# Optimization experiments

Measured on AMD Instinct MI355X. Metric: run time of the kernel, lower is better.

Reference implementation:

```python
import jax, jax.numpy as jnp
import numpy as np

B, T, H, K = 128, 4096, 128, 5


def logistic_logcdf(x, mean, log_scale):
    z = (x - mean) * jnp.exp(-log_scale)
    return jax.nn.log_sigmoid(z)


def logistic_logpdf(x, mean, log_scale):
    z = (x - mean) * jnp.exp(-log_scale)
    zh = z / 2
    return -2 * jnp.logaddexp(zh, -zh) - log_scale


def mixlogistic_logcdf(x, prior_logits, means, log_scales):
    x = x[..., None]
    log_pi = jax.nn.log_softmax(prior_logits, axis=-1)
    return jax.nn.logsumexp(log_pi + logistic_logcdf(x, means, log_scales), axis=-1)


def mixlogistic_logpdf(x, prior_logits, means, log_scales):
    x = x[..., None]
    log_pi = jax.nn.log_softmax(prior_logits, axis=-1)
    return jax.nn.logsumexp(log_pi + logistic_logpdf(x, means, log_scales), axis=-1)


def coupling_function(x, pi, mu, log_s):
    log_cdf = jnp.minimum(mixlogistic_logcdf(x, pi, mu, log_s), -1e-12)
    log_1m = jnp.log(-jnp.expm1(log_cdf))
    val = log_cdf - log_1m
    log_jac = mixlogistic_logpdf(x, pi, mu, log_s) - log_cdf - log_1m
    return val, log_jac


def gru_step(h, x, Wi, Wh, bi, bhn):
    # flax GRUCell: input denses have bias, hidden denses no bias except hn.
    gi = x @ Wi + bi                      # [B, 3H]
    gh = h @ Wh                           # [B, 3H]
    ir, iz, inn = jnp.split(gi, 3, axis=-1)
    hr, hz, hn = jnp.split(gh, 3, axis=-1)
    r = jax.nn.sigmoid(ir + hr)
    z = jax.nn.sigmoid(iz + hz)
    n = jnp.tanh(inn + r * (hn + bhn))
    return (1.0 - z) * n + z * h


def setup_inputs() -> dict:
    key = jax.random.key(0)
    ks = jax.random.split(key, 14)
    g = lambda i, shape: (jax.random.normal(ks[i], shape) * 0.08).astype(jnp.float32)
    return {
        's': jax.random.normal(ks[0], (B, T), jnp.float32),
        'x': jax.random.normal(ks[1], (B, T), jnp.float32),
        'eps': jax.random.logistic(ks[2], (B, T), jnp.float32),
        # encoder GRU (in_features=1)
        'Wi_e': g(3, (1, 3 * H)), 'Wh_e': g(4, (H, 3 * H)),
        'bi_e': jnp.zeros(3 * H, jnp.float32), 'bhn_e': jnp.zeros(H, jnp.float32),
        # decoder GRU (in_features=1+H)
        'Wi_d': g(5, (1 + H, 3 * H)), 'Wh_d': g(6, (H, 3 * H)),
        'bi_d': jnp.zeros(3 * H, jnp.float32), 'bhn_d': jnp.zeros(H, jnp.float32),
        # heads
        'W_shift': g(7, (H, 1)), 'b_shift': jnp.zeros(1, jnp.float32),
        'W_lsc': g(8, (H, 1)), 'b_lsc': jnp.zeros(1, jnp.float32),
        'W_pi': g(9, (H, K)), 'b_pi': jnp.zeros(K, jnp.float32),
        'W_mu': g(10, (H, K)), 'b_mu': jnp.zeros(K, jnp.float32),
        'W_ls': g(11, (H, K)), 'b_ls': jnp.zeros(K, jnp.float32),
    }


def reference(s, x, eps, Wi_e, Wh_e, bi_e, bhn_e, Wi_d, Wh_d, bi_d, bhn_d,
              W_shift, b_shift, W_lsc, b_lsc, W_pi, b_pi, W_mu, b_mu, W_ls, b_ls):
    Bn, Tn = s.shape
    Hn = Wh_e.shape[0]
    s3 = s[..., None]  # [B,T,1]
    x3 = x[..., None]

    # --- encoder: reverse GRU, outputs kept in scan (reversed) order ---
    def enc_step(h, xt):
        h = gru_step(h, xt, Wi_e, Wh_e, bi_e, bhn_e)
        return h, h

    x_rev = jnp.flip(x3, axis=1).transpose(1, 0, 2)  # [T,B,1]
    _, h_x = jax.lax.scan(enc_step, jnp.zeros((Bn, Hn), s.dtype), x_rev)
    h_x = h_x.transpose(1, 0, 2)  # [B,T,H]

    sc = jnp.concatenate([s3, h_x], axis=-1)  # [B,T,1+H]

    def dec_step(carry, xs_t):
        h, pred = carry
        inp, e = xs_t              # inp [B,1+H], e [B]
        inp = inp.at[:, 0].set(pred)
        h = gru_step(h, inp, Wi_d, Wh_d, bi_d, bhn_d)
        y = h
        shift = (y @ W_shift + b_shift)[:, 0]
        log_scale = (y @ W_lsc + b_lsc)[:, 0]
        pi = y @ W_pi + b_pi
        mu = y @ W_mu + b_mu
        log_s = y @ W_ls + b_ls
        val, log_jac = coupling_function(e, pi, mu, log_s)
        prediction = shift + val * jnp.exp(log_scale)
        # standard logistic logpdf(e) = -e - 2*softplus(-e)
        logp = (-e - 2 * jax.nn.softplus(-e)) - log_scale - log_jac
        return (h, prediction), (logp, prediction)

    carry0 = (jnp.zeros((Bn, Hn), s.dtype), jnp.zeros(Bn, s.dtype))
    xs = (sc.transpose(1, 0, 2), eps.T)
    _, (logp, preds) = jax.lax.scan(dec_step, carry0, xs)
    return logp.T, preds.T  # each [B,T]
```

## Files before the change

kernel.cpp:

```cpp
#include <hip/hip_runtime.h>
#include <hip/hip_fp16.h>

#define Tn 4096
#define Bn 128
#define Hn 128
#define G3 384
#define NTH 448

typedef unsigned short u16;
typedef unsigned int u32;
typedef _Float16 f16;
typedef _Float16 h2 __attribute__((ext_vector_type(2)));

__device__ __forceinline__ float sigm(float v) { return 1.f / (1.f + __expf(-v)); }
__device__ __forceinline__ float tanh_fast(float v) {
  v = fminf(fmaxf(v, -15.f), 15.f);
  float e = __expf(-2.f * v);
  return (1.f - e) / (1.f + e);
}
__device__ __forceinline__ u16 f2h(float f) { return __half_as_ushort(__float2half(f)); }
__device__ __forceinline__ float h2f(u16 u) { return __half2float(__ushort_as_half(u)); }
__device__ __forceinline__ h2 bch2(u32 v) { union { u32 u; h2 h; } t; t.u = v; return t.h; }
__device__ __forceinline__ u32 bcu32(h2 v) { union { u32 u; h2 h; } t; t.h = v; return t.u; }
__device__ __forceinline__ float fdot2f(h2 a, h2 b, float c) {
  return __builtin_amdgcn_fdot2(a, b, c, false);
}

__global__ __launch_bounds__(NTH, 1) void combo_kernel(
    const float* __restrict__ x, const float* __restrict__ Wi_e,
    const float* __restrict__ Wh_e, const float* __restrict__ bi_e,
    const float* __restrict__ bhn_e, u16* __restrict__ hx,
    float* __restrict__ enc_h,
    const float* __restrict__ eps, const float* __restrict__ Wi_d,
    const float* __restrict__ Wh_d, const float* __restrict__ bhn_d,
    const float* __restrict__ W_shift, const float* __restrict__ b_shift,
    const float* __restrict__ W_lsc, const float* __restrict__ b_lsc,
    const float* __restrict__ W_pi, const float* __restrict__ b_pi,
    const float* __restrict__ W_mu, const float* __restrict__ b_mu,
    const float* __restrict__ W_ls, const float* __restrict__ b_ls,
    const u16* __restrict__ gi_pre, float* __restrict__ out,
    float* __restrict__ dec_h, float* __restrict__ dec_pred,
    int enc_t0, int dec_t0, int Tc)
{
  const int j = threadIdx.x;
  __shared__ __align__(16) f16 Xp[Hn];
  __shared__ __align__(16) float g2[512];
  __shared__ __align__(16) u32 hwlp[17 * 68];
  __shared__ float hbias_l[20];
  __shared__ float pred_s;
  const int bid = blockIdx.x;
  const int jj = (j < 384) ? j : 0;

  if (bid < Bn) {
    if (enc_t0 < 0) return;
    const int b = bid, t0 = enc_t0;
    h2 wp[64];
#pragma unroll
    for (int k = 0; k < 64; ++k) {
      h2 t; t.x = (f16)Wh_e[(2 * k) * G3 + jj]; t.y = (f16)Wh_e[(2 * k + 1) * G3 + jj];
      wp[k] = t;
    }
    float wie = 0.f, bie = 0.f, bhn = 0.f, hm = 0.f;
    if (j < 384) { wie = Wi_e[j]; bie = bi_e[j]; }
    if (j < Hn) {
      bhn = bhn_e[j];
      hm = (t0 == 0) ? 0.f : enc_h[(long)b * Hn + j];
      Xp[j] = (f16)hm;
    }
    __syncthreads();
    const float* xrow = x + (long)b * Tn;
    u16* hxrow = hx + (long)b * Tc * Hn;
    float xt = xrow[Tn - 1 - t0];
    for (int tt = 0; tt < Tc; ++tt) {
      const int t = t0 + tt;
      const int tnext = (t + 1 < Tn) ? (t + 1) : (Tn - 1);
      float xnext = xrow[Tn - 1 - tnext];
      if (j < 384) {
        const uint4* hp = (const uint4*)Xp;
        float a0 = 0.f, a1 = 0.f, a2 = 0.f, a3 = 0.f;
#pragma unroll
        for (int q = 0; q < 16; ++q) {
          uint4 hv = hp[q];
          a0 = fdot2f(bch2(hv.x), wp[4 * q + 0], a0);
          a1 = fdot2f(bch2(hv.y), wp[4 * q + 1], a1);
          a2 = fdot2f(bch2(hv.z), wp[4 * q + 2], a2);
          a3 = fdot2f(bch2(hv.w), wp[4 * q + 3], a3);
        }
        float gh = (a0 + a1) + (a2 + a3);
        float gi = fmaf(xt, wie, bie);
        if (j < 256) g2[j] = gh + gi;
        else { g2[j] = gh; g2[j + 128] = gi; }
      }
      __syncthreads();
      if (j < Hn) {
        float r = sigm(g2[j]);
        float z = sigm(g2[128 + j]);
        float n = tanh_fast(g2[384 + j] + r * (g2[256 + j] + bhn));
        float hn2 = (1.f - z) * n + z * hm;
        hm = hn2;
        Xp[j] = (f16)hn2;
        hxrow[(long)tt * Hn + j] = f2h(hn2);
      }
      xt = xnext;
      __syncthreads();
    }
    if (j < Hn) enc_h[(long)b * Hn + j] = hm;
  } else {
    if (dec_t0 < 0) return;
    const int b = bid - Bn, t0 = dec_t0;
    h2 wp[64];
#pragma unroll
    for (int k = 0; k < 64; ++k) {
      h2 t; t.x = (f16)Wh_d[(2 * k) * G3 + jj]; t.y = (f16)Wh_d[(2 * k + 1) * G3 + jj];
      wp[k] = t;
    }
    float bhn = 0.f, wr0 = 0.f, wz0 = 0.f, wn0 = 0.f, hm = 0.f;
    if (j < Hn) {
      bhn = bhn_d[j];
      wr0 = Wi_d[j];
      wz0 = Wi_d[128 + j];
      wn0 = Wi_d[256 + j];
      hm = (t0 == 0) ? 0.f : dec_h[(long)b * Hn + j];
      Xp[j] = (f16)hm;
    }
    for (int idx = j; idx < 17 * 64; idx += NTH) {
      int o = idx >> 6, k2 = idx & 63;
      int ka = 2 * k2, kb = 2 * k2 + 1;
      float wa, wb;
      if (o == 0) { wa = W_shift[ka]; wb = W_shift[kb]; }
      else if (o == 1) { wa = W_lsc[ka]; wb = W_lsc[kb]; }
      else if (o < 7) { wa = W_pi[ka * 5 + o - 2]; wb = W_pi[kb * 5 + o - 2]; }
      else if (o < 12) { wa = W_mu[ka * 5 + o - 7]; wb = W_mu[kb * 5 + o - 7]; }
      else { wa = W_ls[ka * 5 + o - 12]; wb = W_ls[kb * 5 + o - 12]; }
      h2 t; t.x = (f16)wa; t.y = (f16)wb;
      hwlp[o * 68 + k2] = bcu32(t);
    }
    if (j < 17)
      hbias_l[j] = (j == 0) ? b_shift[0] : (j == 1) ? b_lsc[0] : (j < 7) ? b_pi[j - 2]
                 : (j < 12) ? b_mu[j - 7] : b_ls[j - 12];
    float predreg = (t0 == 0) ? 0.f : dec_pred[b];
    if (j == 384) pred_s = predreg;
    const u16* girow = gi_pre + (long)b * Tc * G3 + jj;
    const float* erow = eps + (long)b * Tn;
    float e_cur = erow[t0];
    u16 gA = 0, gB = 0;
    if (j < 384) { gA = girow[0]; gB = girow[(Tc > 1) ? G3 : 0]; }
    __syncthreads();
    const int lane = j - 384;
    const int ho = lane >> 1, hs = lane & 1;
    float* outlp = out + (long)b * Tn + t0;
    float* outpr = out + (long)Bn * Tn + (long)b * Tn + t0;
    for (int i = 0; i <= Tc; ++i) {
      u16 gC = 0; float e_next = 0.f;
      if (j < 384 && i < Tc) {
        int ip = (i + 2 < Tc) ? i + 2 : Tc - 1;
        gC = girow[(long)ip * G3];
      }
      if (j >= 384 && i < Tc) e_next = erow[t0 + i];
      if (j < 384) {
        if (i < Tc) {
          const uint4* hp = (const uint4*)Xp;
          float a0 = 0.f, a1 = 0.f, a2 = 0.f, a3 = 0.f;
#pragma unroll
          for (int q = 0; q < 16; ++q) {
            uint4 hv = hp[q];
            a0 = fdot2f(bch2(hv.x), wp[4 * q + 0], a0);
            a1 = fdot2f(bch2(hv.y), wp[4 * q + 1], a1);
            a2 = fdot2f(bch2(hv.z), wp[4 * q + 2], a2);
            a3 = fdot2f(bch2(hv.w), wp[4 * q + 3], a3);
          }
          float gh = (a0 + a1) + (a2 + a3);
          float gipre = h2f(gA);
          if (j < 256) g2[j] = gh + gipre;
          else { g2[j] = gh; g2[j + 128] = gipre; }
        }
      } else if (i >= 1) {
        float p = 0.f;
        if (lane < 34) {
          const uint4* hp4 = (const uint4*)Xp;
          const uint4* wr4 = (const uint4*)&hwlp[ho * 68 + hs * 32];
#pragma unroll
          for (int q = 0; q < 8; ++q) {
            uint4 hv = hp4[hs * 8 + q];
            uint4 wv = wr4[q];
            p = fdot2f(bch2(hv.x), bch2(wv.x), p);
            p = fdot2f(bch2(hv.y), bch2(wv.y), p);
            p = fdot2f(bch2(hv.z), bch2(wv.z), p);
            p = fdot2f(bch2(hv.w), bch2(wv.w), p);
          }
        }
        p += __shfl_xor(p, 1);
        float pb = p + hbias_l[lane < 34 ? ho : 0];
        const int lj2 = lane & 7;
        float pi_ = __shfl(pb, 4 + 2 * lj2);
        float mu_ = __shfl(pb, 14 + 2 * lj2);
        float ls_ = __shfl(pb, 24 + 2 * lj2);
        float shiftv = __shfl(pb, 0);
        float lscv = __shfl(pb, 2);
        const bool valid = (lane < 5);
        const float e = e_cur;
        float wexp = valid ? __expf(pi_) : 0.f;
        float zz = (e - mu_) * __expf(-ls_);
        float u = __expf(-fabsf(zz));
        float d = 1.f / (1.f + u);
        float sigp = (zz >= 0.f) ? d : u * d;
        float sigq = (zz >= 0.f) ? u * d : d;
        float pdfl = u * d * d * __expf(-ls_);
        float c = wexp * sigp, m = wexp * sigq, pp = wexp * pdfl, S = wexp;
        c += __shfl_xor(c, 1, 8); m += __shfl_xor(m, 1, 8);
        pp += __shfl_xor(pp, 1, 8); S += __shfl_xor(S, 1, 8);
        c += __shfl_xor(c, 2, 8); m += __shfl_xor(m, 2, 8);
        pp += __shfl_xor(pp, 2, 8); S += __shfl_xor(S, 2, 8);
        c += __shfl_xor(c, 4, 8); m += __shfl_xor(m, 4, 8);
        pp += __shfl_xor(pp, 4, 8); S += __shfl_xor(S, 4, 8);
        if (lane == 0) {
          float logc = __logf(c), logm = __logf(m);
          float val = logc - logm;
          float ljac = __logf(pp) + __logf(S) - logc - logm;
          float prednew = fmaf(val, __expf(lscv), shiftv);
          float sp = fmaxf(-e, 0.f) + log1pf(__expf(-fabsf(e)));
          float logp = (-e - 2.f * sp) - lscv - ljac;
          outlp[i - 1] = logp;
          outpr[i - 1] = prednew;
          pred_s = prednew;
          predreg = prednew;
        }
      }
      __syncthreads();
      if (j < Hn && i < Tc) {
        float pred = pred_s;
        float r = sigm(fmaf(pred, wr0, g2[j]));
        float z = sigm(fmaf(pred, wz0, g2[128 + j]));
        float n = tanh_fast(fmaf(pred, wn0, g2[384 + j]) + r * (g2[256 + j] + bhn));
        float hn2 = (1.f - z) * n + z * hm;
        hm = hn2;
        Xp[j] = (f16)hn2;
      }
      __syncthreads();
      gA = gB; gB = gC; e_cur = e_next;
    }
    if (j < Hn) dec_h[(long)b * Hn + j] = hm;
    if (j == 384) dec_pred[b] = predreg;
  }
}

__global__ __launch_bounds__(256) void gemm_gi(
    const u16* __restrict__ A, const float* __restrict__ Wi_d,
    const float* __restrict__ bi_d, u16* __restrict__ C)
{
  __shared__ __align__(16) float As[16][64];
  __shared__ __align__(16) float Ws[16][64];
  const int tid = threadIdx.x;
  const long m0 = (long)blockIdx.x * 64;
  const int n0 = blockIdx.y * 64;
  const int tx = tid & 15, ty = tid >> 4;
  const int am = tid >> 2, ak = (tid & 3) * 4;
  const int wk = tid >> 4, wn = (tid & 15) * 4;
  float acc[4][4] = {};
  for (int k0 = 0; k0 < Hn; k0 += 16) {
    uint2 a2v = *(const uint2*)(A + (m0 + am) * Hn + k0 + ak);
    float4 w4 = *(const float4*)(Wi_d + (long)(1 + k0 + wk) * G3 + n0 + wn);
    __syncthreads();
    As[ak + 0][am] = h2f((u16)(a2v.x & 0xffffu));
    As[ak + 1][am] = h2f((u16)(a2v.x >> 16));
    As[ak + 2][am] = h2f((u16)(a2v.y & 0xffffu));
    As[ak + 3][am] = h2f((u16)(a2v.y >> 16));
    *(float4*)&Ws[wk][wn] = w4;
    __syncthreads();
#pragma unroll
    for (int kk = 0; kk < 16; ++kk) {
      float4 av = *(const float4*)&As[kk][ty * 4];
      float4 wv = *(const float4*)&Ws[kk][tx * 4];
      float ar[4] = {av.x, av.y, av.z, av.w};
      float wr[4] = {wv.x, wv.y, wv.z, wv.w};
#pragma unroll
      for (int i = 0; i < 4; ++i)
#pragma unroll
        for (int jj = 0; jj < 4; ++jj) acc[i][jj] = fmaf(ar[i], wr[jj], acc[i][jj]);
    }
  }
  const float4 bb = *(const float4*)(bi_d + n0 + tx * 4);
  const float br[4] = {bb.x, bb.y, bb.z, bb.w};
#pragma unroll
  for (int i = 0; i < 4; ++i) {
    long row = m0 + ty * 4 + i;
    u32 lo = (u32)f2h(acc[i][0] + br[0]) | ((u32)f2h(acc[i][1] + br[1]) << 16);
    u32 hi = (u32)f2h(acc[i][2] + br[2]) | ((u32)f2h(acc[i][3] + br[3]) << 16);
    uint2 o; o.x = lo; o.y = hi;
    *(uint2*)(C + row * G3 + n0 + tx * 4) = o;
  }
}

extern "C" void kernel_launch(void* const* d_in, const int* in_sizes, int n_in,
                              void* d_out, int out_size, void* d_ws, size_t ws_size,
                              hipStream_t stream) {
  const float* x = (const float*)d_in[1];
  const float* eps = (const float*)d_in[2];
  const float* Wi_e = (const float*)d_in[3];
  const float* Wh_e = (const float*)d_in[4];
  const float* bi_e = (const float*)d_in[5];
  const float* bhn_e = (const float*)d_in[6];
  const float* Wi_d = (const float*)d_in[7];
  const float* Wh_d = (const float*)d_in[8];
  const float* bi_d = (const float*)d_in[9];
  const float* bhn_d = (const float*)d_in[10];
  const float* W_shift = (const float*)d_in[11];
  const float* b_shift = (const float*)d_in[12];
  const float* W_lsc = (const float*)d_in[13];
  const float* b_lsc = (const float*)d_in[14];
  const float* W_pi = (const float*)d_in[15];
  const float* b_pi = (const float*)d_in[16];
  const float* W_mu = (const float*)d_in[17];
  const float* b_mu = (const float*)d_in[18];
  const float* W_ls = (const float*)d_in[19];
  const float* b_ls = (const float*)d_in[20];
  float* out = (float*)d_out;

  const size_t stateB = (size_t)(2 * Bn * Hn + Bn) * sizeof(float);
  const size_t stateAl = (stateB + 255) & ~(size_t)255;
  int Tc = 512;
  while (Tc > 8 && stateAl + (size_t)Bn * Tc * (Hn + G3) * 2 > ws_size) Tc >>= 1;
  if (stateAl + (size_t)Bn * Tc * (Hn + G3) * 2 > ws_size) return;

  float* enc_h = (float*)d_ws;
  float* dec_h = enc_h + (size_t)Bn * Hn;
  float* dec_pred = dec_h + (size_t)Bn * Hn;
  u16* hx = (u16*)((char*)d_ws + stateAl);
  u16* gi = hx + (size_t)Bn * Tc * Hn;

  const int Nc = Tn / Tc;
  const dim3 gg((unsigned)(((size_t)Bn * Tc) / 64), G3 / 64);
  for (int k = 0; k <= Nc; ++k) {
    int enc_t0 = (k < Nc) ? k * Tc : -1;
    int dec_t0 = (k >= 1) ? (k - 1) * Tc : -1;
    combo_kernel<<<2 * Bn, NTH, 0, stream>>>(
        x, Wi_e, Wh_e, bi_e, bhn_e, hx, enc_h,
        eps, Wi_d, Wh_d, bhn_d, W_shift, b_shift, W_lsc, b_lsc,
        W_pi, b_pi, W_mu, b_mu, W_ls, b_ls,
        gi, out, dec_h, dec_pred, enc_t0, dec_t0, Tc);
    if (k < Nc) gemm_gi<<<gg, 256, 0, stream>>>(hx, Wi_d, bi_d, gi);
  }
}
```

Before: 6.230 ms.

## Transpose hx and gi buffers to time-major per feature and batch sequential loads by eight

The encoder hidden-state buffer and the precomputed decoder input-gate buffer are stored time-contiguous per (batch, feature) instead of feature-contiguous per timestep. Encoder and decoder loops now run in chunks of 8 steps, so each thread does one 16-byte load or store per 8 steps for x, eps, hx, gi and outputs, rather than scattered 2-byte and 4-byte accesses every step. The GEMM is adapted to read and write the transposed layouts. This adds register pressure from the unrolled 8-step bodies and raises the minimum chunk size to 64.

```diff
diff --git a/kernel.cpp b/kernel.cpp
--- a/kernel.cpp
+++ b/kernel.cpp
@@ -38,7 +38,7 @@
     const float* __restrict__ W_pi, const float* __restrict__ b_pi,
     const float* __restrict__ W_mu, const float* __restrict__ b_mu,
     const float* __restrict__ W_ls, const float* __restrict__ b_ls,
-    const u16* __restrict__ gi_pre, float* __restrict__ out,
+    const u16* __restrict__ gi2, float* __restrict__ out,
     float* __restrict__ dec_h, float* __restrict__ dec_pred,
     int enc_t0, int dec_t0, int Tc)
 {
@@ -67,42 +67,64 @@
       hm = (t0 == 0) ? 0.f : enc_h[(long)b * Hn + j];
       Xp[j] = (f16)hm;
     }
+    const float* xrow = x + (long)b * Tn;
+    u16* hxrow2 = hx + ((long)b * Hn + (j < Hn ? j : 0)) * Tc;
+    float xc0, xc1, xc2, xc3, xc4, xc5, xc6, xc7;
+    {
+      int base = Tn - 8 - t0; if (base < 0) base = 0;
+      float4 v0 = *(const float4*)(xrow + base), v1 = *(const float4*)(xrow + base + 4);
+      xc0 = v1.w; xc1 = v1.z; xc2 = v1.y; xc3 = v1.x;
+      xc4 = v0.w; xc5 = v0.z; xc6 = v0.y; xc7 = v0.x;
+    }
     __syncthreads();
-    const float* xrow = x + (long)b * Tn;
-    u16* hxrow = hx + (long)b * Tc * Hn;
-    float xt = xrow[Tn - 1 - t0];
-    for (int tt = 0; tt < Tc; ++tt) {
-      const int t = t0 + tt;
-      const int tnext = (t + 1 < Tn) ? (t + 1) : (Tn - 1);
-      float xnext = xrow[Tn - 1 - tnext];
-      if (j < 384) {
-        const uint4* hp = (const uint4*)Xp;
-        float a0 = 0.f, a1 = 0.f, a2 = 0.f, a3 = 0.f;
-#pragma unroll
-        for (int q = 0; q < 16; ++q) {
-          uint4 hv = hp[q];
-          a0 = fdot2f(bch2(hv.x), wp[4 * q + 0], a0);
-          a1 = fdot2f(bch2(hv.y), wp[4 * q + 1], a1);
-          a2 = fdot2f(bch2(hv.z), wp[4 * q + 2], a2);
-          a3 = fdot2f(bch2(hv.w), wp[4 * q + 3], a3);
+    for (int i8 = 0; i8 < Tc; i8 += 8) {
+      int nbase = Tn - 8 - t0 - (i8 + 8); if (nbase < 0) nbase = 0;
+      float4 nv0 = *(const float4*)(xrow + nbase);
+      float4 nv1 = *(const float4*)(xrow + nbase + 4);
+      u32 hb0_ = 0, hb1_ = 0, hb2_ = 0, hb3_ = 0;
+#pragma unroll
+      for (int u = 0; u < 8; ++u) {
+        const float xt = (u == 0) ? xc0 : (u == 1) ? xc1 : (u == 2) ? xc2
+                        : (u == 3) ? xc3 : (u == 4) ? xc4 : (u == 5) ? xc5
+                        : (u == 6) ? xc6 : xc7;
+        if (j < 384) {
+          const uint4* hp = (const uint4*)Xp;
+          float a0 = 0.f, a1 = 0.f, a2 = 0.f, a3 = 0.f;
+#pragma unroll
+          for (int q = 0; q < 16; ++q) {
+            uint4 hv = hp[q];
+            a0 = fdot2f(bch2(hv.x), wp[4 * q + 0], a0);
+            a1 = fdot2f(bch2(hv.y), wp[4 * q + 1], a1);
+            a2 = fdot2f(bch2(hv.z), wp[4 * q + 2], a2);
+            a3 = fdot2f(bch2(hv.w), wp[4 * q + 3], a3);
+          }
+          float gh = (a0 + a1) + (a2 + a3);
+          float gi = fmaf(xt, wie, bie);
+          if (j < 256) g2[j] = gh + gi;
+          else { g2[j] = gh; g2[j + 128] = gi; }
         }
-        float gh = (a0 + a1) + (a2 + a3);
-        float gi = fmaf(xt, wie, bie);
-        if (j < 256) g2[j] = gh + gi;
-        else { g2[j] = gh; g2[j + 128] = gi; }
-      }
-      __syncthreads();
+        __syncthreads();
+        if (j < Hn) {
+          float r = sigm(g2[j]);
+          float z = sigm(g2[128 + j]);
+          float n = tanh_fast(g2[384 + j] + r * (g2[256 + j] + bhn));
+          float hn2 = (1.f - z) * n + z * hm;
+          hm = hn2;
+          Xp[j] = (f16)hn2;
+          u16 hv = f2h(hn2);
+          if (u == 0) hb0_ = hv; else if (u == 1) hb0_ |= ((u32)hv << 16);
+          else if (u == 2) hb1_ = hv; else if (u == 3) hb1_ |= ((u32)hv << 16);
+          else if (u == 4) hb2_ = hv; else if (u == 5) hb2_ |= ((u32)hv << 16);
+          else if (u == 6) hb3_ = hv; else hb3_ |= ((u32)hv << 16);
+        }
+        __syncthreads();
+      }
       if (j < Hn) {
-        float r = sigm(g2[j]);
-        float z = sigm(g2[128 + j]);
-        float n = tanh_fast(g2[384 + j] + r * (g2[256 + j] + bhn));
-        float hn2 = (1.f - z) * n + z * hm;
-        hm = hn2;
-        Xp[j] = (f16)hn2;
-        hxrow[(long)tt * Hn + j] = f2h(hn2);
-      }
-      xt = xnext;
-      __syncthreads();
+        uint4 o; o.x = hb0_; o.y = hb1_; o.z = hb2_; o.w = hb3_;
+        *(uint4*)(hxrow2 + i8) = o;
+      }
+      xc0 = nv1.w; xc1 = nv1.z; xc2 = nv1.y; xc3 = nv1.x;
+      xc4 = nv0.w; xc5 = nv0.z; xc6 = nv0.y; xc7 = nv0.x;
     }
     if (j < Hn) enc_h[(long)b * Hn + j] = hm;
   } else {
@@ -140,25 +162,87 @@
                  : (j < 12) ? b_mu[j - 7] : b_ls[j - 12];
     float predreg = (t0 == 0) ? 0.f : dec_pred[b];
     if (j == 384) pred_s = predreg;
-    const u16* girow = gi_pre + (long)b * Tc * G3 + jj;
+    const u16* girow2 = gi2 + ((long)b * G3 + jj) * Tc;
     const float* erow = eps + (long)b * Tn;
-    float e_cur = erow[t0];
-    u16 gA = 0, gB = 0;
-    if (j < 384) { gA = girow[0]; gB = girow[(Tc > 1) ? G3 : 0]; }
+    uint4 gA4 = {0, 0, 0, 0};
+    float ep = 0.f, ec0 = 0, ec1 = 0, ec2 = 0, ec3 = 0, ec4 = 0, ec5 = 0, ec6 = 0, ec7 = 0;
+    if (j < 384) {
+      gA4 = *(const uint4*)(girow2);
+    } else {
+      float4 v0 = *(const float4*)(erow + t0), v1 = *(const float4*)(erow + t0 + 4);
+      ec0 = v0.x; ec1 = v0.y; ec2 = v0.z; ec3 = v0.w;
+      ec4 = v1.x; ec5 = v1.y; ec6 = v1.z; ec7 = v1.w;
+    }
+    float lp0 = 0, lp1 = 0, lp2 = 0, lp3 = 0, lp4 = 0, lp5 = 0, lp6 = 0, lp7 = 0;
+    float pr0 = 0, pr1 = 0, pr2 = 0, pr3 = 0, pr4 = 0, pr5 = 0, pr6 = 0, pr7 = 0;
     __syncthreads();
     const int lane = j - 384;
     const int ho = lane >> 1, hs = lane & 1;
     float* outlp = out + (long)b * Tn + t0;
     float* outpr = out + (long)Bn * Tn + (long)b * Tn + t0;
-    for (int i = 0; i <= Tc; ++i) {
-      u16 gC = 0; float e_next = 0.f;
-      if (j < 384 && i < Tc) {
-        int ip = (i + 2 < Tc) ? i + 2 : Tc - 1;
-        gC = girow[(long)ip * G3];
-      }
-      if (j >= 384 && i < Tc) e_next = erow[t0 + i];
+
+    auto couple = [&](float e) -> float2 {
+      float p = 0.f;
+      if (lane < 34) {
+        const uint4* hp4 = (const uint4*)Xp;
+        const uint4* wr4 = (const uint4*)&hwlp[ho * 68 + hs * 32];
+#pragma unroll
+        for (int q = 0; q < 8; ++q) {
+          uint4 hv = hp4[hs * 8 + q];
+          uint4 wv = wr4[q];
+          p = fdot2f(bch2(hv.x), bch2(wv.x), p);
+          p = fdot2f(bch2(hv.y), bch2(wv.y), p);
+          p = fdot2f(bch2(hv.z), bch2(wv.z), p);
+          p = fdot2f(bch2(hv.w), bch2(wv.w), p);
+        }
+      }
+      p += __shfl_xor(p, 1);
+      float pb = p + hbias_l[lane < 34 ? ho : 0];
+      const int lj2 = lane & 7;
+      float pi_ = __shfl(pb, 4 + 2 * lj2);
+      float mu_ = __shfl(pb, 14 + 2 * lj2);
+      float ls_ = __shfl(pb, 24 + 2 * lj2);
+      float shiftv = __shfl(pb, 0);
+      float lscv = __shfl(pb, 2);
+      const bool valid = (lane < 5);
+      float wexp = valid ? __expf(pi_) : 0.f;
+      float zz = (e - mu_) * __expf(-ls_);
+      float uq = __expf(-fabsf(zz));
+      float dq = 1.f / (1.f + uq);
+      float sigp = (zz >= 0.f) ? dq : uq * dq;
+      float sigq = (zz >= 0.f) ? uq * dq : dq;
+      float pdfl = uq * dq * dq * __expf(-ls_);
+      float c = wexp * sigp, m = wexp * sigq, pq = wexp * pdfl, S = wexp;
+      c += __shfl_xor(c, 1, 8); m += __shfl_xor(m, 1, 8);
+      pq += __shfl_xor(pq, 1, 8); S += __shfl_xor(S, 1, 8);
+      c += __shfl_xor(c, 2, 8); m += __shfl_xor(m, 2, 8);
+      pq += __shfl_xor(pq, 2, 8); S += __shfl_xor(S, 2, 8);
+      c += __shfl_xor(c, 4, 8); m += __shfl_xor(m, 4, 8);
+      pq += __shfl_xor(pq, 4, 8); S += __shfl_xor(S, 4, 8);
+      float logc = __logf(c), logm = __logf(m);
+      float val = logc - logm;
+      float ljac = __logf(pq) + __logf(S) - logc - logm;
+      float prednew = fmaf(val, __expf(lscv), shiftv);
+      float sp = fmaxf(-e, 0.f) + log1pf(__expf(-fabsf(e)));
+      float logp = (-e - 2.f * sp) - lscv - ljac;
+      return make_float2(logp, prednew);
+    };
+
+    for (int i8 = 0; i8 < Tc; i8 += 8) {
+      uint4 gB4 = {0, 0, 0, 0};
+      float4 en0 = {0, 0, 0, 0}, en1 = {0, 0, 0, 0};
       if (j < 384) {
-        if (i < Tc) {
+        int gn = i8 + 8; if (gn > Tc - 8) gn = Tc - 8;
+        gB4 = *(const uint4*)(girow2 + gn);
+      } else {
+        int sn = t0 + i8 + 8; if (sn > Tn - 8) sn = Tn - 8;
+        en0 = *(const float4*)(erow + sn);
+        en1 = *(const float4*)(erow + sn + 4);
+      }
+#pragma unroll
+      for (int u = 0; u < 8; ++u) {
+        const int i = i8 + u;
+        if (j < 384) {
           const uint4* hp = (const uint4*)Xp;
           float a0 = 0.f, a1 = 0.f, a2 = 0.f, a3 = 0.f;
 #pragma unroll
@@ -170,74 +254,64 @@
             a3 = fdot2f(bch2(hv.w), wp[4 * q + 3], a3);
           }
           float gh = (a0 + a1) + (a2 + a3);
-          float gipre = h2f(gA);
+          u16 gv = (u == 0) ? (u16)gA4.x : (u == 1) ? (u16)(gA4.x >> 16)
+                 : (u == 2) ? (u16)gA4.y : (u == 3) ? (u16)(gA4.y >> 16)
+                 : (u == 4) ? (u16)gA4.z : (u == 5) ? (u16)(gA4.z >> 16)
+                 : (u == 6) ? (u16)gA4.w : (u16)(gA4.w >> 16);
+          float gipre = h2f(gv);
           if (j < 256) g2[j] = gh + gipre;
           else { g2[j] = gh; g2[j + 128] = gipre; }
-        }
-      } else if (i >= 1) {
-        float p = 0.f;
-        if (lane < 34) {
-          const uint4* hp4 = (const uint4*)Xp;
-          const uint4* wr4 = (const uint4*)&hwlp[ho * 68 + hs * 32];
-#pragma unroll
-          for (int q = 0; q < 8; ++q) {
-            uint4 hv = hp4[hs * 8 + q];
-            uint4 wv = wr4[q];
-            p = fdot2f(bch2(hv.x), bch2(wv.x), p);
-            p = fdot2f(bch2(hv.y), bch2(wv.y), p);
-            p = fdot2f(bch2(hv.z), bch2(wv.z), p);
-            p = fdot2f(bch2(hv.w), bch2(wv.w), p);
+        } else if (i >= 1) {
+          float e = (u == 0) ? ep : (u == 1) ? ec0 : (u == 2) ? ec1 : (u == 3) ? ec2
+                  : (u == 4) ? ec3 : (u == 5) ? ec4 : (u == 6) ? ec5 : ec6;
+          float2 rr = couple(e);
+          if (lane == 0) {
+            if (u == 0) { lp7 = rr.x; pr7 = rr.y; }
+            else if (u == 1) { lp0 = rr.x; pr0 = rr.y; }
+            else if (u == 2) { lp1 = rr.x; pr1 = rr.y; }
+            else if (u == 3) { lp2 = rr.x; pr2 = rr.y; }
+            else if (u == 4) { lp3 = rr.x; pr3 = rr.y; }
+            else if (u == 5) { lp4 = rr.x; pr4 = rr.y; }
+            else if (u == 6) { lp5 = rr.x; pr5 = rr.y; }
+            else { lp6 = rr.x; pr6 = rr.y; }
+            pred_s = rr.y;
+            predreg = rr.y;
+            if (u == 0 && i8 > 0) {
+              *(float4*)(outlp + i8 - 8) = make_float4(lp0, lp1, lp2, lp3);
+              *(float4*)(outlp + i8 - 4) = make_float4(lp4, lp5, lp6, lp7);
+              *(float4*)(outpr + i8 - 8) = make_float4(pr0, pr1, pr2, pr3);
+              *(float4*)(outpr + i8 - 4) = make_float4(pr4, pr5, pr6, pr7);
+            }
           }
         }
-        p += __shfl_xor(p, 1);
-        float pb = p + hbias_l[lane < 34 ? ho : 0];
-        const int lj2 = lane & 7;
-        float pi_ = __shfl(pb, 4 + 2 * lj2);
-        float mu_ = __shfl(pb, 14 + 2 * lj2);
-        float ls_ = __shfl(pb, 24 + 2 * lj2);
-        float shiftv = __shfl(pb, 0);
-        float lscv = __shfl(pb, 2);
-        const bool valid = (lane < 5);
-        const float e = e_cur;
-        float wexp = valid ? __expf(pi_) : 0.f;
-        float zz = (e - mu_) * __expf(-ls_);
-        float u = __expf(-fabsf(zz));
-        float d = 1.f / (1.f + u);
-        float sigp = (zz >= 0.f) ? d : u * d;
-        float sigq = (zz >= 0.f) ? u * d : d;
-        float pdfl = u * d * d * __expf(-ls_);
-        float c = wexp * sigp, m = wexp * sigq, pp = wexp * pdfl, S = wexp;
-        c += __shfl_xor(c, 1, 8); m += __shfl_xor(m, 1, 8);
-        pp += __shfl_xor(pp, 1, 8); S += __shfl_xor(S, 1, 8);
-        c += __shfl_xor(c, 2, 8); m += __shfl_xor(m, 2, 8);
-        pp += __shfl_xor(pp, 2, 8); S += __shfl_xor(S, 2, 8);
-        c += __shfl_xor(c, 4, 8); m += __shfl_xor(m, 4, 8);
-        pp += __shfl_xor(pp, 4, 8); S += __shfl_xor(S, 4, 8);
-        if (lane == 0) {
-          float logc = __logf(c), logm = __logf(m);
-          float val = logc - logm;
-          float ljac = __logf(pp) + __logf(S) - logc - logm;
-          float prednew = fmaf(val, __expf(lscv), shiftv);
-          float sp = fmaxf(-e, 0.f) + log1pf(__expf(-fabsf(e)));
-          float logp = (-e - 2.f * sp) - lscv - ljac;
-          outlp[i - 1] = logp;
-          outpr[i - 1] = prednew;
-          pred_s = prednew;
-          predreg = prednew;
+        __syncthreads();
+        if (j < Hn) {
+          float pred = pred_s;
+          float r = sigm(fmaf(pred, wr0, g2[j]));
+          float z = sigm(fmaf(pred, wz0, g2[128 + j]));
+          float n = tanh_fast(fmaf(pred, wn0, g2[384 + j]) + r * (g2[256 + j] + bhn));
+          float hn2 = (1.f - z) * n + z * hm;
+          hm = hn2;
+          Xp[j] = (f16)hn2;
         }
-      }
-      __syncthreads();
-      if (j < Hn && i < Tc) {
-        float pred = pred_s;
-        float r = sigm(fmaf(pred, wr0, g2[j]));
-        float z = sigm(fmaf(pred, wz0, g2[128 + j]));
-        float n = tanh_fast(fmaf(pred, wn0, g2[384 + j]) + r * (g2[256 + j] + bhn));
-        float hn2 = (1.f - z) * n + z * hm;
-        hm = hn2;
-        Xp[j] = (f16)hn2;
-      }
-      __syncthreads();
-      gA = gB; gB = gC; e_cur = e_next;
+        __syncthreads();
+      }
+      gA4 = gB4;
+      if (j >= 384) {
+        ep = ec7;
+        ec0 = en0.x; ec1 = en0.y; ec2 = en0.z; ec3 = en0.w;
+        ec4 = en1.x; ec5 = en1.y; ec6 = en1.z; ec7 = en1.w;
+      }
+    }
+    if (j >= 384) {
+      float2 rr = couple(ep);
+      if (lane == 0) {
+        lp7 = rr.x; pr7 = rr.y; predreg = rr.y;
+        *(float4*)(outlp + Tc - 8) = make_float4(lp0, lp1, lp2, lp3);
+        *(float4*)(outlp + Tc - 4) = make_float4(lp4, lp5, lp6, lp7);
+        *(float4*)(outpr + Tc - 8) = make_float4(pr0, pr1, pr2, pr3);
+        *(float4*)(outpr + Tc - 4) = make_float4(pr4, pr5, pr6, pr7);
+      }
     }
     if (j < Hn) dec_h[(long)b * Hn + j] = hm;
     if (j == 384) dec_pred[b] = predreg;
@@ -245,26 +319,28 @@
 }
 
 __global__ __launch_bounds__(256) void gemm_gi(
-    const u16* __restrict__ A, const float* __restrict__ Wi_d,
-    const float* __restrict__ bi_d, u16* __restrict__ C)
+    const u16* __restrict__ A2, const float* __restrict__ Wi_d,
+    const float* __restrict__ bi_d, u16* __restrict__ C2, int Tc)
 {
   __shared__ __align__(16) float As[16][64];
   __shared__ __align__(16) float Ws[16][64];
   const int tid = threadIdx.x;
   const long m0 = (long)blockIdx.x * 64;
   const int n0 = blockIdx.y * 64;
+  const int bb = (int)(m0 / Tc);
+  const int tt0 = (int)(m0 - (long)bb * Tc);
   const int tx = tid & 15, ty = tid >> 4;
-  const int am = tid >> 2, ak = (tid & 3) * 4;
+  const int lk = tid >> 4, lm = (tid & 15) * 4;
   const int wk = tid >> 4, wn = (tid & 15) * 4;
   float acc[4][4] = {};
   for (int k0 = 0; k0 < Hn; k0 += 16) {
-    uint2 a2v = *(const uint2*)(A + (m0 + am) * Hn + k0 + ak);
+    uint2 a2v = *(const uint2*)(A2 + ((long)bb * Hn + k0 + lk) * Tc + tt0 + lm);
     float4 w4 = *(const float4*)(Wi_d + (long)(1 + k0 + wk) * G3 + n0 + wn);
     __syncthreads();
-    As[ak + 0][am] = h2f((u16)(a2v.x & 0xffffu));
-    As[ak + 1][am] = h2f((u16)(a2v.x >> 16));
-    As[ak + 2][am] = h2f((u16)(a2v.y & 0xffffu));
-    As[ak + 3][am] = h2f((u16)(a2v.y >> 16));
+    As[lk][lm + 0] = h2f((u16)(a2v.x & 0xffffu));
+    As[lk][lm + 1] = h2f((u16)(a2v.x >> 16));
+    As[lk][lm + 2] = h2f((u16)(a2v.y & 0xffffu));
+    As[lk][lm + 3] = h2f((u16)(a2v.y >> 16));
     *(float4*)&Ws[wk][wn] = w4;
     __syncthreads();
 #pragma unroll
@@ -279,15 +355,15 @@
         for (int jj = 0; jj < 4; ++jj) acc[i][jj] = fmaf(ar[i], wr[jj], acc[i][jj]);
     }
   }
-  const float4 bb = *(const float4*)(bi_d + n0 + tx * 4);
-  const float br[4] = {bb.x, bb.y, bb.z, bb.w};
-#pragma unroll
-  for (int i = 0; i < 4; ++i) {
-    long row = m0 + ty * 4 + i;
-    u32 lo = (u32)f2h(acc[i][0] + br[0]) | ((u32)f2h(acc[i][1] + br[1]) << 16);
-    u32 hi = (u32)f2h(acc[i][2] + br[2]) | ((u32)f2h(acc[i][3] + br[3]) << 16);
+  const float4 bbv = *(const float4*)(bi_d + n0 + tx * 4);
+  const float br[4] = {bbv.x, bbv.y, bbv.z, bbv.w};
+#pragma unroll
+  for (int jj = 0; jj < 4; ++jj) {
+    int colc = n0 + tx * 4 + jj;
+    u32 lo = (u32)f2h(acc[0][jj] + br[jj]) | ((u32)f2h(acc[1][jj] + br[jj]) << 16);
+    u32 hi = (u32)f2h(acc[2][jj] + br[jj]) | ((u32)f2h(acc[3][jj] + br[jj]) << 16);
     uint2 o; o.x = lo; o.y = hi;
-    *(uint2*)(C + row * G3 + n0 + tx * 4) = o;
+    *(uint2*)(C2 + ((long)bb * G3 + colc) * Tc + tt0 + ty * 4) = o;
   }
 }
 
@@ -319,7 +395,7 @@
   const size_t stateB = (size_t)(2 * Bn * Hn + Bn) * sizeof(float);
   const size_t stateAl = (stateB + 255) & ~(size_t)255;
   int Tc = 512;
-  while (Tc > 8 && stateAl + (size_t)Bn * Tc * (Hn + G3) * 2 > ws_size) Tc >>= 1;
+  while (Tc > 64 && stateAl + (size_t)Bn * Tc * (Hn + G3) * 2 > ws_size) Tc >>= 1;
   if (stateAl + (size_t)Bn * Tc * (Hn + G3) * 2 > ws_size) return;
 
   float* enc_h = (float*)d_ws;
@@ -338,6 +414,6 @@
         eps, Wi_d, Wh_d, bhn_d, W_shift, b_shift, W_lsc, b_lsc,
         W_pi, b_pi, W_mu, b_mu, W_ls, b_ls,
         gi, out, dec_h, dec_pred, enc_t0, dec_t0, Tc);
-    if (k < Nc) gemm_gi<<<gg, 256, 0, stream>>>(hx, Wi_d, bi_d, gi);
+    if (k < Nc) gemm_gi<<<gg, 256, 0, stream>>>(hx, Wi_d, bi_d, gi, Tc);
   }
 }
```

New measurement: 5.793 ms. -7.0%, faster.
